# Optimization experiments

Hardware: AMD Instinct MI355X
Metric: run time of the kernel (lower is better)

Reference implementation:

```python
import jax, jax.numpy as jnp
import numpy as np

N, C, L, K = 150000, 256, 50000, 200  # nodes, classes(=feature dim), labeled count, top-k


def setup_inputs() -> dict:
    key = jax.random.key(0)
    k1, k2 = jax.random.split(key)
    inputs = jax.random.normal(k1, (N, C), dtype=jnp.float32)
    cls = jax.random.randint(k2, (N,), 0, C)
    labels = jax.nn.one_hot(cls, C, dtype=jnp.float32)  # one-hot label matrix [N, C]
    labels_mask = jnp.arange(N) < L      # first L nodes labeled
    unlabels_mask = ~labels_mask
    return {"inputs": inputs, "labels": labels, "labels_mask": labels_mask,
            "unlabels_mask": unlabels_mask, "k": K}


def _l2n(x):
    # tf.nn.l2_normalize with epsilon 1e-12
    return x * jax.lax.rsqrt(jnp.maximum(jnp.sum(x * x, axis=-1, keepdims=True), 1e-12))


def reference(inputs, labels, labels_mask, unlabels_mask, k):
    lm = labels_mask.astype(inputs.dtype)    # [N]
    um = unlabels_mask.astype(inputs.dtype)  # [N]
    # protos: per-class mean of labeled features (masked matmul == boolean_mask + matmul)
    total = jnp.einsum('nf,nc->fc', inputs * lm[:, None], labels)  # [F, C]
    weight = 1.0 / jnp.sum(labels, 0)                               # 1/count per class (over ALL labels, as in TF)
    protos = (total * weight[None, :]).T                            # [C, F]
    # cosine similarity of every node to every prototype [N, C]
    prob = _l2n(inputs) @ _l2n(protos).T
    # per-row top-k, scattered back to a sparse [N, C] (raw top values, softmax in TF was dead code)
    vals, idx = jax.lax.top_k(prob, k)                              # [N, k]
    rows = jnp.arange(prob.shape[0])[:, None]
    sparse = jnp.zeros_like(prob).at[rows, idx].set(vals)
    p = sparse * um[:, None]                                        # only unlabeled rows contribute
    # per-class normalization: denom_c = sum_u p[u,c] + n_labeled_c
    denom = jnp.sum(p, 0) + jnp.sum(labels * lm[:, None], 0)        # [C]
    w = p / denom[None, :]                                          # [N, C]
    # change[c] = sum_u w[u,c] * (x_u - protos[c])
    change = w.T @ inputs - jnp.sum(w, 0)[:, None] * protos         # [C, F]
    protos = protos + change
    logits = _l2n(inputs) @ _l2n(protos).T                          # [N, C]
    return logits
```

## Files before the change

### kernel.cpp

```cpp
#include <hip/hip_runtime.h>

typedef unsigned int uint;
typedef unsigned short ushort;
typedef float f32x4 __attribute__((ext_vector_type(4)));
typedef uint u32x4 __attribute__((ext_vector_type(4)));
typedef uint u32x2 __attribute__((ext_vector_type(2)));
typedef __bf16 bf16x8 __attribute__((ext_vector_type(8)));

constexpr int NR = 150000;
constexpr int CD = 256;
constexpr int LR = 50000;
constexpr int KEX = 56;
constexpr int NB1 = 49984;
constexpr int NUP = 100032;
constexpr int NTP = 150080;

__device__ __forceinline__ ushort f2bf(float x) {
  uint u = __builtin_bit_cast(uint, x);
  u += 0x7FFFu + ((u >> 16) & 1u);
  return (ushort)(u >> 16);
}
__device__ __forceinline__ uint key16(uint b) {
  return (b & 0x8000u) ? (~b & 0xFFFFu) : (b | 0x8000u);
}

__global__ __launch_bounds__(256) void k_cls(const float* __restrict__ labels,
                                             int* __restrict__ cls,
                                             float* __restrict__ ca,
                                             float* __restrict__ cl) {
  __shared__ int ha[256], hl[256];
  int t = threadIdx.x;
  ha[t] = 0; hl[t] = 0;
  __syncthreads();
  int lane = t & 63;
  int wid = (blockIdx.x << 2) | (t >> 6);
  int nw = gridDim.x << 2;
  int n = wid;
  for (; n + 3 * nw < NR; n += 4 * nw) {
    f32x4 v[4];
#pragma unroll
    for (int u = 0; u < 4; ++u)
      v[u] = *reinterpret_cast<const f32x4*>(&labels[(size_t)(n + u * nw) * CD + lane * 4]);
#pragma unroll
    for (int u = 0; u < 4; ++u) {
      int nn = n + u * nw;
      int j = v[u][0] > 0.5f ? 0 : v[u][1] > 0.5f ? 1 : v[u][2] > 0.5f ? 2
                                                      : v[u][3] > 0.5f ? 3 : -1;
      if (j >= 0) {
        int c = lane * 4 + j;
        cls[nn] = c;
        atomicAdd(&ha[c], 1);
        if (nn < LR) atomicAdd(&hl[c], 1);
      }
    }
  }
  for (; n < NR; n += nw) {
    f32x4 v = *reinterpret_cast<const f32x4*>(&labels[(size_t)n * CD + lane * 4]);
    int j = v[0] > 0.5f ? 0 : v[1] > 0.5f ? 1 : v[2] > 0.5f ? 2 : v[3] > 0.5f ? 3 : -1;
    if (j >= 0) {
      int c = lane * 4 + j;
      cls[n] = c;
      atomicAdd(&ha[c], 1);
      if (n < LR) atomicAdd(&hl[c], 1);
    }
  }
  __syncthreads();
  atomicAdd(&ca[t], (float)ha[t]);
  atomicAdd(&cl[t], (float)hl[t]);
}

__global__ __launch_bounds__(256) void k_prep(const float* __restrict__ X,
                                              ushort* __restrict__ Xt,
                                              float* __restrict__ invn) {
  __shared__ __align__(16) ushort xl[64 * 264];
  __shared__ float red[256];
  int t = threadIdx.x;
  int r = t >> 2, cq = t & 3;
  int g0 = blockIdx.x * 64;
  int g = g0 + r;
  bool valid = g < NR;
  float ss = 0.f;
#pragma unroll
  for (int j = 0; j < 16; ++j) {
    int col = cq * 4 + j * 16;
    f32x4 x = valid ? *reinterpret_cast<const f32x4*>(&X[g * CD + col])
                    : (f32x4){0.f, 0.f, 0.f, 0.f};
    ss += x[0] * x[0] + x[1] * x[1] + x[2] * x[2] + x[3] * x[3];
    uint p0 = (uint)f2bf(x[0]) | ((uint)f2bf(x[1]) << 16);
    uint p1 = (uint)f2bf(x[2]) | ((uint)f2bf(x[3]) << 16);
    *reinterpret_cast<u32x2*>(&xl[r * 264 + col]) = (u32x2){p0, p1};
  }
  red[t] = ss;
  __syncthreads();
  if (t < 64) {
    float s4 = red[t * 4] + red[t * 4 + 1] + red[t * 4 + 2] + red[t * 4 + 3];
    if (g0 + t < NR) invn[g0 + t] = rsqrtf(fmaxf(s4, 1e-12f));
  }
  ushort* xp = Xt + (size_t)blockIdx.x * 16384;
  int f = t;
  uint buf[4];
  for (int n = 0; n < 64; ++n) {
    ushort v16 = xl[n * 264 + f];
    int sl = n & 7;
    if (sl & 1) buf[sl >> 1] |= (uint)v16 << 16; else buf[sl >> 1] = v16;
    if (sl == 7)
      *reinterpret_cast<u32x4*>(&xp[f * 64 + n - 7]) =
          (u32x4){buf[0], buf[1], buf[2], buf[3]};
  }
}

template <int KIND>
__global__ __launch_bounds__(1024) void k_gemmB(const int* __restrict__ cls,
                                                const ushort* __restrict__ Ap,
                                                const ushort* __restrict__ Xt,
                                                float* __restrict__ P,
                                                int nch, int nbase) {
  __shared__ __align__(16) ushort Al[256 * 40];
  __shared__ __align__(16) ushort Bl[256 * 40];
  int t = threadIdx.x;
  int lane = t & 63, w = t >> 6;
  int m = lane & 15, qd = lane >> 4;
  int cR = t >> 2, off = (t & 3) * 8;
  f32x4 acc[16];
#pragma unroll
  for (int i = 0; i < 16; ++i) acc[i] = (f32x4){0.f, 0.f, 0.f, 0.f};

  if (KIND == 0) {
    for (int i = t; i < 5120; i += 1024) reinterpret_cast<uint*>(Al)[i] = 0u;
  }

  u32x4 aR, bR;
  int curc = -1, prevc = -1;
  int ch = blockIdx.x;
  if (ch < nch) {
    int n0 = ch * 32;
    if (KIND == 1) {
      const ushort* ap = Ap + (size_t)(n0 >> 6) * 16384 + (n0 & 63);
      aR = *reinterpret_cast<const u32x4*>(&ap[cR * 64 + off]);
    } else if (t < 32) {
      int gg = n0 + t;
      curc = (gg < LR) ? cls[gg] : -1;
    }
    int gr = nbase + n0;
    const ushort* xp = Xt + (size_t)(gr >> 6) * 16384 + (gr & 63);
    bR = *reinterpret_cast<const u32x4*>(&xp[cR * 64 + off]);
  }

  for (; ch < nch; ch += gridDim.x) {
    __syncthreads();
    if (KIND == 0) {
      if (t < 32) {
        if (prevc >= 0) Al[prevc * 40 + t] = 0;
        if (curc >= 0) Al[curc * 40 + t] = 0x3F80;
        prevc = curc;
      }
    } else {
      *reinterpret_cast<u32x4*>(&Al[cR * 40 + off]) = aR;
    }
    *reinterpret_cast<u32x4*>(&Bl[cR * 40 + off]) = bR;
    int chn = ch + gridDim.x;
    if (chn < nch) {
      int n0 = chn * 32;
      if (KIND == 1) {
        const ushort* ap = Ap + (size_t)(n0 >> 6) * 16384 + (n0 & 63);
        aR = *reinterpret_cast<const u32x4*>(&ap[cR * 64 + off]);
      } else if (t < 32) {
        int gg = n0 + t;
        curc = (gg < LR) ? cls[gg] : -1;
      }
      int gr = nbase + n0;
      const ushort* xp = Xt + (size_t)(gr >> 6) * 16384 + (gr & 63);
      bR = *reinterpret_cast<const u32x4*>(&xp[cR * 64 + off]);
    }
    __syncthreads();
    bf16x8 a = *reinterpret_cast<const bf16x8*>(&Al[(w * 16 + m) * 40 + qd * 8]);
#pragma unroll
    for (int ft = 0; ft < 16; ++ft) {
      bf16x8 b = *reinterpret_cast<const bf16x8*>(&Bl[(ft * 16 + m) * 40 + qd * 8]);
      acc[ft] = __builtin_amdgcn_mfma_f32_16x16x32_bf16(a, b, acc[ft], 0, 0, 0);
    }
  }
  float* Ps = P + (size_t)blockIdx.x * 65536;
#pragma unroll
  for (int ft = 0; ft < 16; ++ft)
#pragma unroll
    for (int r = 0; r < 4; ++r)
      Ps[(w * 16 + qd * 4 + r) * 256 + ft * 16 + m] = acc[ft][r];
}

__global__ __launch_bounds__(256) void k_protos(const float* __restrict__ P, int nsl,
                                                const float* __restrict__ ca,
                                                float* __restrict__ protos,
                                                ushort* __restrict__ phat) {
  __shared__ float red[256];
  int c = blockIdx.x, f = threadIdx.x;
  float s = 0.f;
  for (int i = 0; i < nsl; ++i) s += P[i * 65536 + c * 256 + f];
  float cnt = ca[c];
  float pv = cnt > 0.5f ? s / cnt : 0.f;
  protos[c * 256 + f] = pv;
  red[f] = pv * pv;
  __syncthreads();
  for (int st = 128; st > 0; st >>= 1) {
    if (f < st) red[f] += red[f + st];
    __syncthreads();
  }
  float iv = rsqrtf(fmaxf(red[0], 1e-12f));
  phat[c * 256 + f] = f2bf(pv * iv);
}

__global__ __launch_bounds__(256) void k_update(const float* __restrict__ PS, int nsl,
                                                const float* __restrict__ protos,
                                                const float* __restrict__ q,
                                                const float* __restrict__ clab,
                                                ushort* __restrict__ phat2) {
  __shared__ float red[256];
  int c = blockIdx.x, f = threadIdx.x;
  float s = 0.f;
  for (int i = 0; i < nsl; ++i) s += PS[i * 65536 + c * 256 + f];
  float qc = q[c];
  float den = qc + clab[c];
  float pv = protos[c * 256 + f];
  float np = pv + (s - qc * pv) / den;
  red[f] = np * np;
  __syncthreads();
  for (int st = 128; st > 0; st >>= 1) {
    if (f < st) red[f] += red[f + st];
    __syncthreads();
  }
  float iv = rsqrtf(fmaxf(red[0], 1e-12f));
  phat2[c * 256 + f] = f2bf(np * iv);
}

template <int TOPK>
__global__ __launch_bounds__(256, 4) void k_passA(const float* __restrict__ X,
                                                  const float* __restrict__ invn,
                                                  const ushort* __restrict__ Bm,
                                                  float* __restrict__ out,
                                                  ushort* __restrict__ pt,
                                                  float* __restrict__ q,
                                                  int gbase) {
  __shared__ __align__(16) char smem[TOPK ? 35072 : 20480];
  ushort* Bl = reinterpret_cast<ushort*>(smem);
  int t = threadIdx.x;
  int lane = t & 63, w = t >> 6;
  int m = lane & 15, qd = lane >> 4;
  int g0 = gbase + blockIdx.x * 64;
  int g2 = g0 + w * 16 + m;
  bool vA = g2 < NR;
  float inv2 = vA ? invn[g2] : 0.f;
  const float* xp = X + (size_t)(vA ? g2 : 0) * CD + qd * 8;
  int cB = t >> 2, offB = (t & 3) * 8;
  f32x4 acc[16];
#pragma unroll
  for (int i = 0; i < 16; ++i) acc[i] = (f32x4){0.f, 0.f, 0.f, 0.f};

  f32x4 x0 = *reinterpret_cast<const f32x4*>(&xp[0]);
  f32x4 x1 = *reinterpret_cast<const f32x4*>(&xp[4]);
  u32x4 bR[4];
#pragma unroll
  for (int i = 0; i < 4; ++i)
    bR[i] = *reinterpret_cast<const u32x4*>(&Bm[(cB + i * 64) * 256 + offB]);

  for (int k0 = 0; k0 < 256; k0 += 32) {
    f32x4 y0 = x0 * inv2, y1 = x1 * inv2;
    uint u0 = (uint)f2bf(y0[0]) | ((uint)f2bf(y0[1]) << 16);
    uint u1 = (uint)f2bf(y0[2]) | ((uint)f2bf(y0[3]) << 16);
    uint u2 = (uint)f2bf(y1[0]) | ((uint)f2bf(y1[1]) << 16);
    uint u3 = (uint)f2bf(y1[2]) | ((uint)f2bf(y1[3]) << 16);
    u32x4 au = (u32x4){u0, u1, u2, u3};
    bf16x8 a = __builtin_bit_cast(bf16x8, au);
    __syncthreads();
#pragma unroll
    for (int i = 0; i < 4; ++i)
      *reinterpret_cast<u32x4*>(&Bl[(cB + i * 64) * 40 + offB]) = bR[i];
    if (k0 < 224) {
      int kn = k0 + 32;
      x0 = *reinterpret_cast<const f32x4*>(&xp[kn]);
      x1 = *reinterpret_cast<const f32x4*>(&xp[kn + 4]);
#pragma unroll
      for (int i = 0; i < 4; ++i)
        bR[i] = *reinterpret_cast<const u32x4*>(
            &Bm[(cB + i * 64) * 256 + kn + offB]);
    }
    __syncthreads();
#pragma unroll
    for (int ft = 0; ft < 16; ++ft) {
      bf16x8 b = *reinterpret_cast<const bf16x8*>(&Bl[(ft * 16 + m) * 40 + qd * 8]);
      acc[ft] = __builtin_amdgcn_mfma_f32_16x16x32_bf16(a, b, acc[ft], 0, 0, 0);
    }
  }

  if constexpr (TOPK == 0) {
#pragma unroll
    for (int ft = 0; ft < 16; ++ft)
#pragma unroll
      for (int r = 0; r < 4; ++r) {
        int rr = w * 16 + qd * 4 + r;
        int gg = g0 + rr;
        if (gg < NR) out[gg * 256 + ft * 16 + m] = acc[ft][r];
      }
  } else {
    ushort* s16 = reinterpret_cast<ushort*>(smem);
    uint* tkey = reinterpret_cast<uint*>(smem + 34816);
    __syncthreads();
#pragma unroll
    for (int ft = 0; ft < 16; ++ft)
#pragma unroll
      for (int r = 0; r < 4; ++r)
        s16[(w * 16 + qd * 4 + r) * 272 + ft * 16 + m] = f2bf(acc[ft][r]);
    for (int i0 = 0; i0 < 16; i0 += 4) {
      uint kk[4][4];
      uint mth[4];
#pragma unroll
      for (int rr = 0; rr < 4; ++rr) {
        int rw = w * 16 + i0 + rr;
        u32x2 pk = *reinterpret_cast<const u32x2*>(&s16[rw * 272 + lane * 4]);
        kk[rr][0] = key16(pk[0] & 0xFFFFu);
        kk[rr][1] = key16(pk[0] >> 16);
        kk[rr][2] = key16(pk[1] & 0xFFFFu);
        kk[rr][3] = key16(pk[1] >> 16);
        mth[rr] = 0u;
      }
      for (int b = 15; b >= 0; --b) {
#pragma unroll
        for (int rr = 0; rr < 4; ++rr) {
          uint cand = mth[rr] | (1u << b);
          int cnt = __builtin_popcountll(__ballot(kk[rr][0] < cand)) +
                    __builtin_popcountll(__ballot(kk[rr][1] < cand)) +
                    __builtin_popcountll(__ballot(kk[rr][2] < cand)) +
                    __builtin_popcountll(__ballot(kk[rr][3] < cand));
          if (cnt <= KEX) mth[rr] = cand;
        }
      }
      if (lane == 0) {
#pragma unroll
        for (int rr = 0; rr < 4; ++rr) tkey[w * 16 + i0 + rr] = mth[rr];
      }
    }
    __syncthreads();
    int c = t;
    float qloc = 0.f;
    uint buf[4];
    ushort* pp = pt + (size_t)blockIdx.x * 16384;
    for (int n = 0; n < 64; ++n) {
      int grow = g0 + n;
      ushort v16 = s16[n * 272 + c];
      bool keep = (key16(v16) >= tkey[n]) && (grow >= LR) && (grow < NR);
      ushort pv16 = keep ? v16 : (ushort)0;
      if (keep) qloc += __builtin_bit_cast(float, (uint)v16 << 16);
      int sl = n & 7;
      if (sl & 1) buf[sl >> 1] |= (uint)pv16 << 16; else buf[sl >> 1] = pv16;
      if (sl == 7)
        *reinterpret_cast<u32x4*>(&pp[c * 64 + n - 7]) =
            (u32x4){buf[0], buf[1], buf[2], buf[3]};
    }
    atomicAdd(&q[c], qloc);
  }
}

extern "C" void kernel_launch(void* const* d_in, const int* in_sizes, int n_in,
                              void* d_out, int out_size, void* d_ws, size_t ws_size,
                              hipStream_t stream) {
  const float* inputs = (const float*)d_in[0];
  const float* labels = (const float*)d_in[1];
  float* out = (float*)d_out;

  ushort* p_t = (ushort*)d_out;
  ushort* Xt  = (ushort*)((char*)d_out + (size_t)256 * NUP * 2);

  char* ws = (char*)d_ws;
  float* q      = (float*)(ws + 0);
  float* c_all  = (float*)(ws + 1024);
  float* c_lab  = (float*)(ws + 2048);
  float* protos = (float*)(ws + 4096);
  ushort* phat  = (ushort*)(ws + 4096 + 262144);
  ushort* phat2 = (ushort*)(ws + 4096 + 262144 + 131072);
  float* invn   = (float*)(ws + 528384);
  int*   cls    = (int*)(ws + 1128384);
  size_t base = 1736704;
  int sT = 256, sS = 256;
  while (base + (size_t)(sT + sS) * 262144ULL > ws_size) {
    if (sS > sT) sS >>= 1; else if (sT > 8) sT >>= 1; else break;
  }
  float* PT = (float*)(ws + base);
  float* PS = PT + (size_t)sT * 65536;

  hipMemsetAsync(ws, 0, 3072, stream);

  k_cls<<<1024, 256, 0, stream>>>(labels, cls, c_all, c_lab);
  k_prep<<<NTP / 64, 256, 0, stream>>>(inputs, Xt, invn);
  k_gemmB<0><<<sT, 1024, 0, stream>>>(cls, nullptr, Xt, PT, 1563, 0);
  k_protos<<<256, 256, 0, stream>>>(PT, sT, c_all, protos, phat);
  k_passA<1><<<NUP / 64, 256, 0, stream>>>(inputs, invn, phat, nullptr, p_t, q, NB1);
  k_gemmB<1><<<sS, 1024, 0, stream>>>(nullptr, p_t, Xt, PS, NUP / 32, NB1);
  k_update<<<256, 256, 0, stream>>>(PS, sS, protos, q, c_lab, phat2);
  k_passA<0><<<(NR + 63) / 64, 256, 0, stream>>>(inputs, invn, phat2, out, nullptr, nullptr, 0);
}
```

Baseline: 753.7 us.

## Merge class-count and prep kernels; write top-k output directly from registers

The label histogram kernel and the bf16 transpose/norm prep kernel become one launch, with class-count blocks interleaved among prep blocks by block index, so the two run concurrently and one launch is saved. In the top-k pass, each lane now keeps the thresholds for its own rows in registers and builds the transposed sparse output straight from the MFMA accumulators. Neighbouring lanes pair up through a shuffle to form 16-byte stores, which replaces the serial 64-row scan over shared memory. Per-column sums are accumulated with shared-memory atomics before a single global atomic per column, which adds LDS atomic contention in exchange.

```diff
diff --git a/kernel.cpp b/kernel.cpp
--- a/kernel.cpp
+++ b/kernel.cpp
@@ -14,6 +14,9 @@
 constexpr int NB1 = 49984;
 constexpr int NUP = 100032;
 constexpr int NTP = 150080;
+constexpr int NPB = NTP / 64;
+constexpr int NCB = 1024;
+constexpr int NFB = NPB + NCB;
 
 __device__ __forceinline__ ushort f2bf(float x) {
   uint u = __builtin_bit_cast(uint, x);
@@ -23,89 +26,98 @@
 __device__ __forceinline__ uint key16(uint b) {
   return (b & 0x8000u) ? (~b & 0xFFFFu) : (b | 0x8000u);
 }
-
-__global__ __launch_bounds__(256) void k_cls(const float* __restrict__ labels,
+__device__ __forceinline__ float bfval(uint p) {
+  return __builtin_bit_cast(float, p << 16);
+}
+
+__global__ __launch_bounds__(256) void k_pre(const float* __restrict__ X,
+                                             const float* __restrict__ labels,
+                                             ushort* __restrict__ Xt,
+                                             float* __restrict__ invn,
                                              int* __restrict__ cls,
                                              float* __restrict__ ca,
                                              float* __restrict__ cl) {
-  __shared__ int ha[256], hl[256];
+  __shared__ __align__(16) char sm[34816];
   int t = threadIdx.x;
-  ha[t] = 0; hl[t] = 0;
-  __syncthreads();
-  int lane = t & 63;
-  int wid = (blockIdx.x << 2) | (t >> 6);
-  int nw = gridDim.x << 2;
-  int n = wid;
-  for (; n + 3 * nw < NR; n += 4 * nw) {
-    f32x4 v[4];
-#pragma unroll
-    for (int u = 0; u < 4; ++u)
-      v[u] = *reinterpret_cast<const f32x4*>(&labels[(size_t)(n + u * nw) * CD + lane * 4]);
-#pragma unroll
-    for (int u = 0; u < 4; ++u) {
-      int nn = n + u * nw;
-      int j = v[u][0] > 0.5f ? 0 : v[u][1] > 0.5f ? 1 : v[u][2] > 0.5f ? 2
-                                                      : v[u][3] > 0.5f ? 3 : -1;
+  uint bx = blockIdx.x;
+  uint ia = (bx * (uint)NCB) / (uint)NFB;
+  uint ib = ((bx + 1) * (uint)NCB) / (uint)NFB;
+  if (ib > ia) {
+    int* ha = (int*)sm;
+    int* hl = (int*)(sm + 1024);
+    ha[t] = 0; hl[t] = 0;
+    __syncthreads();
+    int lane = t & 63;
+    int wid = ((int)ia << 2) | (t >> 6);
+    int nw = NCB << 2;
+    int n = wid;
+    for (; n + 3 * nw < NR; n += 4 * nw) {
+      f32x4 v[4];
+#pragma unroll
+      for (int u = 0; u < 4; ++u)
+        v[u] = *reinterpret_cast<const f32x4*>(&labels[(size_t)(n + u * nw) * CD + lane * 4]);
+#pragma unroll
+      for (int u = 0; u < 4; ++u) {
+        int nn = n + u * nw;
+        int j = v[u][0] > 0.5f ? 0 : v[u][1] > 0.5f ? 1 : v[u][2] > 0.5f ? 2
+                                                        : v[u][3] > 0.5f ? 3 : -1;
+        if (j >= 0) {
+          int c = lane * 4 + j;
+          cls[nn] = c;
+          atomicAdd(&ha[c], 1);
+          if (nn < LR) atomicAdd(&hl[c], 1);
+        }
+      }
+    }
+    for (; n < NR; n += nw) {
+      f32x4 v = *reinterpret_cast<const f32x4*>(&labels[(size_t)n * CD + lane * 4]);
+      int j = v[0] > 0.5f ? 0 : v[1] > 0.5f ? 1 : v[2] > 0.5f ? 2 : v[3] > 0.5f ? 3 : -1;
       if (j >= 0) {
         int c = lane * 4 + j;
-        cls[nn] = c;
+        cls[n] = c;
         atomicAdd(&ha[c], 1);
-        if (nn < LR) atomicAdd(&hl[c], 1);
-      }
-    }
-  }
-  for (; n < NR; n += nw) {
-    f32x4 v = *reinterpret_cast<const f32x4*>(&labels[(size_t)n * CD + lane * 4]);
-    int j = v[0] > 0.5f ? 0 : v[1] > 0.5f ? 1 : v[2] > 0.5f ? 2 : v[3] > 0.5f ? 3 : -1;
-    if (j >= 0) {
-      int c = lane * 4 + j;
-      cls[n] = c;
-      atomicAdd(&ha[c], 1);
-      if (n < LR) atomicAdd(&hl[c], 1);
-    }
-  }
-  __syncthreads();
-  atomicAdd(&ca[t], (float)ha[t]);
-  atomicAdd(&cl[t], (float)hl[t]);
-}
-
-__global__ __launch_bounds__(256) void k_prep(const float* __restrict__ X,
-                                              ushort* __restrict__ Xt,
-                                              float* __restrict__ invn) {
-  __shared__ __align__(16) ushort xl[64 * 264];
-  __shared__ float red[256];
-  int t = threadIdx.x;
-  int r = t >> 2, cq = t & 3;
-  int g0 = blockIdx.x * 64;
-  int g = g0 + r;
-  bool valid = g < NR;
-  float ss = 0.f;
-#pragma unroll
-  for (int j = 0; j < 16; ++j) {
-    int col = cq * 4 + j * 16;
-    f32x4 x = valid ? *reinterpret_cast<const f32x4*>(&X[g * CD + col])
-                    : (f32x4){0.f, 0.f, 0.f, 0.f};
-    ss += x[0] * x[0] + x[1] * x[1] + x[2] * x[2] + x[3] * x[3];
-    uint p0 = (uint)f2bf(x[0]) | ((uint)f2bf(x[1]) << 16);
-    uint p1 = (uint)f2bf(x[2]) | ((uint)f2bf(x[3]) << 16);
-    *reinterpret_cast<u32x2*>(&xl[r * 264 + col]) = (u32x2){p0, p1};
-  }
-  red[t] = ss;
-  __syncthreads();
-  if (t < 64) {
-    float s4 = red[t * 4] + red[t * 4 + 1] + red[t * 4 + 2] + red[t * 4 + 3];
-    if (g0 + t < NR) invn[g0 + t] = rsqrtf(fmaxf(s4, 1e-12f));
-  }
-  ushort* xp = Xt + (size_t)blockIdx.x * 16384;
-  int f = t;
-  uint buf[4];
-  for (int n = 0; n < 64; ++n) {
-    ushort v16 = xl[n * 264 + f];
-    int sl = n & 7;
-    if (sl & 1) buf[sl >> 1] |= (uint)v16 << 16; else buf[sl >> 1] = v16;
-    if (sl == 7)
-      *reinterpret_cast<u32x4*>(&xp[f * 64 + n - 7]) =
-          (u32x4){buf[0], buf[1], buf[2], buf[3]};
+        if (n < LR) atomicAdd(&hl[c], 1);
+      }
+    }
+    __syncthreads();
+    atomicAdd(&ca[t], (float)ha[t]);
+    atomicAdd(&cl[t], (float)hl[t]);
+  } else {
+    int pb = (int)(bx - ia);
+    ushort* xl = (ushort*)sm;
+    float* red = (float*)(sm + 33792);
+    int r = t >> 2, cq = t & 3;
+    int g0 = pb * 64;
+    int g = g0 + r;
+    bool valid = g < NR;
+    float ss = 0.f;
+#pragma unroll
+    for (int j = 0; j < 16; ++j) {
+      int col = cq * 4 + j * 16;
+      f32x4 x = valid ? *reinterpret_cast<const f32x4*>(&X[g * CD + col])
+                      : (f32x4){0.f, 0.f, 0.f, 0.f};
+      ss += x[0] * x[0] + x[1] * x[1] + x[2] * x[2] + x[3] * x[3];
+      uint p0 = (uint)f2bf(x[0]) | ((uint)f2bf(x[1]) << 16);
+      uint p1 = (uint)f2bf(x[2]) | ((uint)f2bf(x[3]) << 16);
+      *reinterpret_cast<u32x2*>(&xl[r * 264 + col]) = (u32x2){p0, p1};
+    }
+    red[t] = ss;
+    __syncthreads();
+    if (t < 64) {
+      float s4 = red[t * 4] + red[t * 4 + 1] + red[t * 4 + 2] + red[t * 4 + 3];
+      if (g0 + t < NR) invn[g0 + t] = rsqrtf(fmaxf(s4, 1e-12f));
+    }
+    ushort* xp = Xt + (size_t)pb * 16384;
+    int f = t;
+    uint buf[4];
+    for (int n = 0; n < 64; ++n) {
+      ushort v16 = xl[n * 264 + f];
+      int sl = n & 7;
+      if (sl & 1) buf[sl >> 1] |= (uint)v16 << 16; else buf[sl >> 1] = v16;
+      if (sl == 7)
+        *reinterpret_cast<u32x4*>(&xp[f * 64 + n - 7]) =
+            (u32x4){buf[0], buf[1], buf[2], buf[3]};
+    }
   }
 }
 
@@ -240,8 +252,9 @@
                                                   ushort* __restrict__ pt,
                                                   float* __restrict__ q,
                                                   int gbase) {
-  __shared__ __align__(16) char smem[TOPK ? 35072 : 20480];
+  __shared__ __align__(16) char smem[TOPK ? 35840 : 20480];
   ushort* Bl = reinterpret_cast<ushort*>(smem);
+  float* qlds = reinterpret_cast<float*>(smem + 34816);
   int t = threadIdx.x;
   int lane = t & 63, w = t >> 6;
   int m = lane & 15, qd = lane >> 4;
@@ -251,6 +264,7 @@
   float inv2 = vA ? invn[g2] : 0.f;
   const float* xp = X + (size_t)(vA ? g2 : 0) * CD + qd * 8;
   int cB = t >> 2, offB = (t & 3) * 8;
+  if (TOPK) qlds[t] = 0.f;
   f32x4 acc[16];
 #pragma unroll
   for (int i = 0; i < 16; ++i) acc[i] = (f32x4){0.f, 0.f, 0.f, 0.f};
@@ -302,13 +316,13 @@
       }
   } else {
     ushort* s16 = reinterpret_cast<ushort*>(smem);
-    uint* tkey = reinterpret_cast<uint*>(smem + 34816);
     __syncthreads();
 #pragma unroll
     for (int ft = 0; ft < 16; ++ft)
 #pragma unroll
       for (int r = 0; r < 4; ++r)
         s16[(w * 16 + qd * 4 + r) * 272 + ft * 16 + m] = f2bf(acc[ft][r]);
+    uint tk0 = 0, tk1 = 0, tk2 = 0, tk3 = 0;
     for (int i0 = 0; i0 < 16; i0 += 4) {
       uint kk[4][4];
       uint mth[4];
@@ -333,29 +347,34 @@
           if (cnt <= KEX) mth[rr] = cand;
         }
       }
-      if (lane == 0) {
-#pragma unroll
-        for (int rr = 0; rr < 4; ++rr) tkey[w * 16 + i0 + rr] = mth[rr];
-      }
-    }
-    __syncthreads();
-    int c = t;
-    float qloc = 0.f;
-    uint buf[4];
+      if (i0 == (qd << 2)) { tk0 = mth[0]; tk1 = mth[1]; tk2 = mth[2]; tk3 = mth[3]; }
+    }
+    int brow = g0 + w * 16 + qd * 4;
+    bool ok0 = (brow + 0 >= LR) && (brow + 0 < NR);
+    bool ok1 = (brow + 1 >= LR) && (brow + 1 < NR);
+    bool ok2 = (brow + 2 >= LR) && (brow + 2 < NR);
+    bool ok3 = (brow + 3 >= LR) && (brow + 3 < NR);
     ushort* pp = pt + (size_t)blockIdx.x * 16384;
-    for (int n = 0; n < 64; ++n) {
-      int grow = g0 + n;
-      ushort v16 = s16[n * 272 + c];
-      bool keep = (key16(v16) >= tkey[n]) && (grow >= LR) && (grow < NR);
-      ushort pv16 = keep ? v16 : (ushort)0;
-      if (keep) qloc += __builtin_bit_cast(float, (uint)v16 << 16);
-      int sl = n & 7;
-      if (sl & 1) buf[sl >> 1] |= (uint)pv16 << 16; else buf[sl >> 1] = pv16;
-      if (sl == 7)
-        *reinterpret_cast<u32x4*>(&pp[c * 64 + n - 7]) =
-            (u32x4){buf[0], buf[1], buf[2], buf[3]};
-    }
-    atomicAdd(&q[c], qloc);
+#pragma unroll
+    for (int ft = 0; ft < 16; ++ft) {
+      uint v0 = f2bf(acc[ft][0]), v1 = f2bf(acc[ft][1]);
+      uint v2 = f2bf(acc[ft][2]), v3 = f2bf(acc[ft][3]);
+      uint p0 = (ok0 && key16(v0) >= tk0) ? v0 : 0u;
+      uint p1 = (ok1 && key16(v1) >= tk1) ? v1 : 0u;
+      uint p2 = (ok2 && key16(v2) >= tk2) ? v2 : 0u;
+      uint p3 = (ok3 && key16(v3) >= tk3) ? v3 : 0u;
+      uint lo = p0 | (p1 << 16), hi = p2 | (p3 << 16);
+      float qv = bfval(p0) + bfval(p1) + bfval(p2) + bfval(p3);
+      uint plo = __shfl_xor(lo, 16);
+      uint phi = __shfl_xor(hi, 16);
+      if (qd & 1)
+        *reinterpret_cast<u32x4*>(
+            &pp[(ft * 16 + m) * 64 + w * 16 + (qd >> 1) * 8]) =
+            (u32x4){plo, phi, lo, hi};
+      atomicAdd(&qlds[ft * 16 + m], qv);
+    }
+    __syncthreads();
+    atomicAdd(&q[t], qlds[t]);
   }
 }
 
@@ -388,8 +407,7 @@
 
   hipMemsetAsync(ws, 0, 3072, stream);
 
-  k_cls<<<1024, 256, 0, stream>>>(labels, cls, c_all, c_lab);
-  k_prep<<<NTP / 64, 256, 0, stream>>>(inputs, Xt, invn);
+  k_pre<<<NFB, 256, 0, stream>>>(inputs, labels, Xt, invn, cls, c_all, c_lab);
   k_gemmB<0><<<sT, 1024, 0, stream>>>(cls, nullptr, Xt, PT, 1563, 0);
   k_protos<<<256, 256, 0, stream>>>(PT, sT, c_all, protos, phat);
   k_passA<1><<<NUP / 64, 256, 0, stream>>>(inputs, invn, phat, nullptr, p_t, q, NB1);
```

Result: faster. 717.9 us (-4.8%).
